# Kernel optimization log

Hardware: AMD Instinct MI355X
Metric: run time of the kernel (lower is better)

Reference implementation:

```python
import jax, jax.numpy as jnp
import numpy as np


def setup_inputs() -> dict:
    key = jax.random.key(0)
    k1, k2 = jax.random.split(key)
    yhat = jax.random.normal(k1, (64, 128, 4096), dtype=jnp.float32)
    y = jax.random.normal(k2, (64, 128, 4096), dtype=jnp.float32)
    return {"yhat": yhat, "y": y}


def reference(yhat, y):
    # Original: sum over (batch, dim) of mean(|yhat[i,j] - y[i,j]|), divided by batch*dim.
    # All slices have identical size, so this equals the global L1 mean.
    return jnp.mean(jnp.abs(yhat - y))
```

## Files before the change

### kernel.cpp

```cpp
#include <hip/hip_runtime.h>

#define NBLOCKS 2048
#define NTHREADS 256

__global__ __launch_bounds__(NTHREADS) void l1_partial_kernel(
    const float4* __restrict__ a, const float4* __restrict__ b,
    float* __restrict__ partial, long n4) {
    long idx = (long)blockIdx.x * blockDim.x + threadIdx.x;
    long stride = (long)gridDim.x * blockDim.x;
    float acc = 0.0f;
    for (long i = idx; i < n4; i += stride) {
        float4 x = a[i];
        float4 y = b[i];
        acc += fabsf(x.x - y.x);
        acc += fabsf(x.y - y.y);
        acc += fabsf(x.z - y.z);
        acc += fabsf(x.w - y.w);
    }
    #pragma unroll
    for (int off = 32; off > 0; off >>= 1)
        acc += __shfl_down(acc, off, 64);
    __shared__ float smem[NTHREADS / 64];
    int wave = threadIdx.x >> 6;
    int lane = threadIdx.x & 63;
    if (lane == 0) smem[wave] = acc;
    __syncthreads();
    if (threadIdx.x == 0) {
        float s = 0.0f;
        #pragma unroll
        for (int w = 0; w < NTHREADS / 64; ++w) s += smem[w];
        partial[blockIdx.x] = s;
    }
}

__global__ __launch_bounds__(NTHREADS) void l1_final_kernel(
    const float* __restrict__ partial, int nblocks,
    const float* __restrict__ a_tail, const float* __restrict__ b_tail,
    long tail_start, long n_total, float* __restrict__ out) {
    float acc = 0.0f;
    for (int i = threadIdx.x; i < nblocks; i += blockDim.x)
        acc += partial[i];
    for (long i = tail_start + threadIdx.x; i < n_total; i += blockDim.x)
        acc += fabsf(a_tail[i] - b_tail[i]);
    #pragma unroll
    for (int off = 32; off > 0; off >>= 1)
        acc += __shfl_down(acc, off, 64);
    __shared__ float smem[NTHREADS / 64];
    int wave = threadIdx.x >> 6;
    int lane = threadIdx.x & 63;
    if (lane == 0) smem[wave] = acc;
    __syncthreads();
    if (threadIdx.x == 0) {
        float s = 0.0f;
        #pragma unroll
        for (int w = 0; w < NTHREADS / 64; ++w) s += smem[w];
        out[0] = s / (float)n_total;
    }
}

extern "C" void kernel_launch(void* const* d_in, const int* in_sizes, int n_in,
                              void* d_out, int out_size, void* d_ws, size_t ws_size,
                              hipStream_t stream) {
    const float* yhat = (const float*)d_in[0];
    const float* y    = (const float*)d_in[1];
    float* out = (float*)d_out;
    float* partial = (float*)d_ws;

    long n = (long)in_sizes[0];
    long n4 = n / 4;
    long tail_start = n4 * 4;

    l1_partial_kernel<<<NBLOCKS, NTHREADS, 0, stream>>>(
        (const float4*)yhat, (const float4*)y, partial, n4);
    l1_final_kernel<<<1, NTHREADS, 0, stream>>>(
        partial, NBLOCKS, yhat, y, tail_start, n, out);
}
```

Measured before the change: 277.0 us.

## Fuse L1 reduction into one kernel with atomic finish and 4-way unrolled loads

```diff
diff --git a/kernel.cpp b/kernel.cpp
--- a/kernel.cpp
+++ b/kernel.cpp
@@ -3,58 +3,58 @@
 #define NBLOCKS 2048
 #define NTHREADS 256
 
-__global__ __launch_bounds__(NTHREADS) void l1_partial_kernel(
+__global__ __launch_bounds__(NTHREADS) void l1_fused_kernel(
     const float4* __restrict__ a, const float4* __restrict__ b,
-    float* __restrict__ partial, long n4) {
-    long idx = (long)blockIdx.x * blockDim.x + threadIdx.x;
-    long stride = (long)gridDim.x * blockDim.x;
-    float acc = 0.0f;
-    for (long i = idx; i < n4; i += stride) {
+    const float* __restrict__ af, const float* __restrict__ bf,
+    float* __restrict__ out, long n4, long n_total, float inv_n) {
+    const long gid = (long)blockIdx.x * NTHREADS + threadIdx.x;
+    const long stride = (long)NBLOCKS * NTHREADS;
+
+    float acc0 = 0.f, acc1 = 0.f, acc2 = 0.f, acc3 = 0.f;
+    long i = gid;
+    for (; i + 3 * stride < n4; i += 4 * stride) {
+        float4 x0 = a[i];
+        float4 x1 = a[i + stride];
+        float4 x2 = a[i + 2 * stride];
+        float4 x3 = a[i + 3 * stride];
+        float4 y0 = b[i];
+        float4 y1 = b[i + stride];
+        float4 y2 = b[i + 2 * stride];
+        float4 y3 = b[i + 3 * stride];
+        acc0 += fabsf(x0.x - y0.x) + fabsf(x0.y - y0.y) +
+                fabsf(x0.z - y0.z) + fabsf(x0.w - y0.w);
+        acc1 += fabsf(x1.x - y1.x) + fabsf(x1.y - y1.y) +
+                fabsf(x1.z - y1.z) + fabsf(x1.w - y1.w);
+        acc2 += fabsf(x2.x - y2.x) + fabsf(x2.y - y2.y) +
+                fabsf(x2.z - y2.z) + fabsf(x2.w - y2.w);
+        acc3 += fabsf(x3.x - y3.x) + fabsf(x3.y - y3.y) +
+                fabsf(x3.z - y3.z) + fabsf(x3.w - y3.w);
+    }
+    for (; i < n4; i += stride) {
         float4 x = a[i];
         float4 y = b[i];
-        acc += fabsf(x.x - y.x);
-        acc += fabsf(x.y - y.y);
-        acc += fabsf(x.z - y.z);
-        acc += fabsf(x.w - y.w);
+        acc0 += fabsf(x.x - y.x) + fabsf(x.y - y.y) +
+                fabsf(x.z - y.z) + fabsf(x.w - y.w);
     }
+    for (long e = n4 * 4 + gid; e < n_total; e += stride)
+        acc0 += fabsf(af[e] - bf[e]);
+
+    float acc = (acc0 + acc1) + (acc2 + acc3);
+
     #pragma unroll
     for (int off = 32; off > 0; off >>= 1)
         acc += __shfl_down(acc, off, 64);
+
     __shared__ float smem[NTHREADS / 64];
     int wave = threadIdx.x >> 6;
     int lane = threadIdx.x & 63;
     if (lane == 0) smem[wave] = acc;
     __syncthreads();
     if (threadIdx.x == 0) {
-        float s = 0.0f;
+        float s = 0.f;
         #pragma unroll
         for (int w = 0; w < NTHREADS / 64; ++w) s += smem[w];
-        partial[blockIdx.x] = s;
-    }
-}
-
-__global__ __launch_bounds__(NTHREADS) void l1_final_kernel(
-    const float* __restrict__ partial, int nblocks,
-    const float* __restrict__ a_tail, const float* __restrict__ b_tail,
-    long tail_start, long n_total, float* __restrict__ out) {
-    float acc = 0.0f;
-    for (int i = threadIdx.x; i < nblocks; i += blockDim.x)
-        acc += partial[i];
-    for (long i = tail_start + threadIdx.x; i < n_total; i += blockDim.x)
-        acc += fabsf(a_tail[i] - b_tail[i]);
-    #pragma unroll
-    for (int off = 32; off > 0; off >>= 1)
-        acc += __shfl_down(acc, off, 64);
-    __shared__ float smem[NTHREADS / 64];
-    int wave = threadIdx.x >> 6;
-    int lane = threadIdx.x & 63;
-    if (lane == 0) smem[wave] = acc;
-    __syncthreads();
-    if (threadIdx.x == 0) {
-        float s = 0.0f;
-        #pragma unroll
-        for (int w = 0; w < NTHREADS / 64; ++w) s += smem[w];
-        out[0] = s / (float)n_total;
+        atomicAdd(out, s * inv_n);
     }
 }
 
@@ -64,14 +64,12 @@
     const float* yhat = (const float*)d_in[0];
     const float* y    = (const float*)d_in[1];
     float* out = (float*)d_out;
-    float* partial = (float*)d_ws;
 
     long n = (long)in_sizes[0];
     long n4 = n / 4;
-    long tail_start = n4 * 4;
+    float inv_n = 1.0f / (float)n;
 
-    l1_partial_kernel<<<NBLOCKS, NTHREADS, 0, stream>>>(
-        (const float4*)yhat, (const float4*)y, partial, n4);
-    l1_final_kernel<<<1, NTHREADS, 0, stream>>>(
-        partial, NBLOCKS, yhat, y, tail_start, n, out);
+    hipMemsetAsync(out, 0, sizeof(float), stream);
+    l1_fused_kernel<<<NBLOCKS, NTHREADS, 0, stream>>>(
+        (const float4*)yhat, (const float4*)y, yhat, y, out, n4, n, inv_n);
 }
```

Result: no change. 275.3 us (-0.6%).
